# Kernel tuning notes

Hardware: AMD Instinct MI355X
Metric: run time of the kernel (lower is better)

## Reference

```python
import jax, jax.numpy as jnp
import numpy as np

B, N_CAM, D_BINS, HF, WF, C = 1, 6, 118, 32, 88, 80
DZ, DY, DX = 1, 128, 128
N_POINTS = 1_000_000
BEV_FEAT_SHAPE = (B, DZ, DY, DX, C)  # (B, Dz, Dy, Dx, C)


def setup_inputs() -> dict:
    key = jax.random.key(0)
    k1, k2, k3, k4, k5 = jax.random.split(key, 5)
    depth = jax.random.uniform(k1, (B, N_CAM, D_BINS, HF, WF), dtype=jnp.float32)
    feat = jax.random.normal(k2, (B, N_CAM, HF, WF, C), dtype=jnp.float32)
    n_depth = B * N_CAM * D_BINS * HF * WF      # flattened depth size
    n_feat_rows = B * N_CAM * HF * WF           # rows of flattened feat
    n_bev = B * DZ * DY * DX                    # flattened BEV grid size
    ranks_depths = jax.random.randint(k3, (N_POINTS,), 0, n_depth, dtype=jnp.int32)
    ranks_feats = jax.random.randint(k4, (N_POINTS,), 0, n_feat_rows, dtype=jnp.int32)
    ranks_bevs = jnp.sort(jax.random.randint(k5, (N_POINTS,), 0, n_bev, dtype=jnp.int32))
    # intervals consistent with sorted ranks_bevs (contiguous runs of equal bev rank)
    rb = np.asarray(ranks_bevs)
    change = np.concatenate([[True], rb[1:] != rb[:-1]])
    starts = np.flatnonzero(change)
    lengths = np.diff(np.append(starts, len(rb)))
    return {
        "depth": depth,
        "feat": feat,
        "ranks_depths": ranks_depths,
        "ranks_feats": ranks_feats,
        "ranks_bevs": ranks_bevs,
        "bev_feat_shape": BEV_FEAT_SHAPE,
        "interval_starts": jnp.asarray(starts, dtype=jnp.int32),
        "interval_lengths": jnp.asarray(lengths, dtype=jnp.int32),
    }


def reference(depth, feat, ranks_depths, ranks_feats, ranks_bevs,
              bev_feat_shape, interval_starts, interval_lengths):
    # bev_pool_v2: gather depth scalar and feat row per point, multiply,
    # scatter-sum into the BEV grid. Interval-based summation over sorted
    # ranks_bevs is mathematically a segment-sum keyed by ranks_bevs, so we
    # use segment_sum directly (intervals are redundant metadata).
    b, dz, dy, dx, c = bev_feat_shape
    d = depth.reshape(-1)[ranks_depths]               # [P]
    f = feat.reshape(-1, c)[ranks_feats]              # [P, C]
    out = jax.ops.segment_sum(f * d[:, None], ranks_bevs,
                              num_segments=b * dz * dy * dx)  # [B*Dz*Dy*Dx, C]
    out = out.reshape(b, dz, dy, dx, c)
    return jnp.transpose(out, (0, 4, 1, 2, 3))        # (B, C, Dz, Dy, Dx)
```

## Files before the change

kernel.cpp:

```cpp
#include <hip/hip_runtime.h>
#include <hip/hip_bf16.h>


#define C_CH   80
#define QPT    20
#define SPLITS 8
#define IPB    2
#define BLOCK  (IPB * QPT * SPLITS)

__global__ __launch_bounds__(BLOCK) void bev_pool_split_kernel(
    const float*  __restrict__ depth,
    const float4* __restrict__ feat4,
    const int*    __restrict__ rd,
    const int*    __restrict__ rf,
    const int*    __restrict__ rb,
    const int*    __restrict__ istart,
    const int*    __restrict__ ilen,
    int n_intervals,
    int n_bev,
    float* __restrict__ out)
{
    __shared__ float4 red[IPB][SPLITS][QPT];

    int tid   = threadIdx.x;
    int il    = tid / (QPT * SPLITS);
    int r     = tid - il * (QPT * SPLITS);
    int split = r / QPT;
    int quad  = r - split * QPT;
    int interval = blockIdx.x * IPB + il;
    bool valid = interval < n_intervals;

    float4 acc = make_float4(0.f, 0.f, 0.f, 0.f);
    int start = 0, len = 0, bev = 0;

    if (valid) {
        start = istart[interval];
        len   = ilen[interval];
        bev   = rb[start];

        int i = split;
        for (; i + SPLITS < len; i += 2 * SPLITS) {
            int p0 = start + i;
            int p1 = p0 + SPLITS;
            int rd0 = rd[p0], rf0 = rf[p0];
            int rd1 = rd[p1], rf1 = rf[p1];
            float d0 = depth[rd0];
            float d1 = depth[rd1];
            float4 f0 = feat4[(long)rf0 * QPT + quad];
            float4 f1 = feat4[(long)rf1 * QPT + quad];
            acc.x += d0 * f0.x; acc.y += d0 * f0.y;
            acc.z += d0 * f0.z; acc.w += d0 * f0.w;
            acc.x += d1 * f1.x; acc.y += d1 * f1.y;
            acc.z += d1 * f1.z; acc.w += d1 * f1.w;
        }
        if (i < len) {
            int p = start + i;
            float d = depth[rd[p]];
            float4 f = feat4[(long)rf[p] * QPT + quad];
            acc.x += d * f.x; acc.y += d * f.y;
            acc.z += d * f.z; acc.w += d * f.w;
        }
    }

    red[il][split][quad] = acc;
    __syncthreads();

    if (valid && split == 0) {
        float4 s = acc;
        #pragma unroll
        for (int k = 1; k < SPLITS; ++k) {
            float4 t = red[il][k][quad];
            s.x += t.x; s.y += t.y; s.z += t.z; s.w += t.w;
        }
        long o = (long)(quad * 4) * n_bev + bev;
        out[o]             = s.x;
        out[o + n_bev]     = s.y;
        out[o + 2L * n_bev] = s.z;
        out[o + 3L * n_bev] = s.w;
    }
}

extern "C" void kernel_launch(void* const* d_in, const int* in_sizes, int n_in,
                              void* d_out, int out_size, void* d_ws, size_t ws_size,
                              hipStream_t stream) {
    const float*  depth = (const float*)d_in[0];
    const float4* feat4 = (const float4*)d_in[1];
    const int* ranks_depth = (const int*)d_in[2];
    const int* ranks_feat  = (const int*)d_in[3];
    const int* ranks_bev   = (const int*)d_in[4];
    const int* interval_starts  = (const int*)d_in[6];
    const int* interval_lengths = (const int*)d_in[7];

    int n_intervals = in_sizes[6];
    int n_bev = out_size / C_CH;
    float* out = (float*)d_out;

    hipMemsetAsync(d_out, 0, (size_t)out_size * sizeof(float), stream);

    int grid = (n_intervals + IPB - 1) / IPB;
    bev_pool_split_kernel<<<grid, BLOCK, 0, stream>>>(
        depth, feat4, ranks_depth, ranks_feat, ranks_bev,
        interval_starts, interval_lengths, n_intervals, n_bev, out);
}
```

Before: 134.9 us.

## Pre-gather depth values and split channels across blocks in clustered grid

Adds a separate kernel that gathers depth values per point into a contiguous workspace buffer, so the main kernel reads them coalesced instead of doing a dependent random gather. The main kernel now splits the 80 channels into two halves handled by different blocks, with 4 intervals per block. Blocks are arranged in clusters of 8 so that neighbouring blocks share intervals and can reuse index data through cache. This adds an extra kernel launch and a P-sized write and read, and it duplicates the index and depth reads across the two channel halves.

```diff
diff --git a/kernel.cpp b/kernel.cpp
--- a/kernel.cpp
+++ b/kernel.cpp
@@ -4,14 +4,25 @@
 
 #define C_CH   80
 #define QPT    20
+#define HQ     10
 #define SPLITS 8
-#define IPB    2
-#define BLOCK  (IPB * QPT * SPLITS)
+#define IPB    4
+#define BLOCK  (IPB * SPLITS * HQ)
+#define CLUST  (IPB * 4)
 
-__global__ __launch_bounds__(BLOCK) void bev_pool_split_kernel(
+__global__ void depth_gather_kernel(const float* __restrict__ depth,
+                                    const int*   __restrict__ rd,
+                                    float* __restrict__ dgath, int P) {
+    int i = blockIdx.x * blockDim.x + threadIdx.x;
+    if (i < P) dgath[i] = depth[rd[i]];
+}
+
+template <bool USE_DG>
+__global__ __launch_bounds__(BLOCK) void bev_pool_main_kernel(
     const float*  __restrict__ depth,
+    const float*  __restrict__ dgath,
+    const int*    __restrict__ rd,
     const float4* __restrict__ feat4,
-    const int*    __restrict__ rd,
     const int*    __restrict__ rf,
     const int*    __restrict__ rb,
     const int*    __restrict__ istart,
@@ -20,34 +31,42 @@
     int n_bev,
     float* __restrict__ out)
 {
-    __shared__ float4 red[IPB][SPLITS][QPT];
+    __shared__ float4 red[IPB][SPLITS][HQ];
+
+    int bid     = blockIdx.x;
+    int slot    = bid & 7;
+    int cluster = bid >> 3;
+    int half    = slot >> 2;
+    int quarter = slot & 3;
+    int ibase   = cluster * CLUST + quarter * IPB;
 
     int tid   = threadIdx.x;
-    int il    = tid / (QPT * SPLITS);
-    int r     = tid - il * (QPT * SPLITS);
-    int split = r / QPT;
-    int quad  = r - split * QPT;
-    int interval = blockIdx.x * IPB + il;
+    int il    = tid / (SPLITS * HQ);
+    int r     = tid - il * (SPLITS * HQ);
+    int split = r / HQ;
+    int q     = r - split * HQ;
+    int gq    = half * HQ + q;
+
+    int interval = ibase + il;
     bool valid = interval < n_intervals;
 
     float4 acc = make_float4(0.f, 0.f, 0.f, 0.f);
-    int start = 0, len = 0, bev = 0;
+    int bev = 0;
 
     if (valid) {
-        start = istart[interval];
-        len   = ilen[interval];
-        bev   = rb[start];
+        int start = istart[interval];
+        int len   = ilen[interval];
+        bev = rb[start];
 
         int i = split;
         for (; i + SPLITS < len; i += 2 * SPLITS) {
             int p0 = start + i;
             int p1 = p0 + SPLITS;
-            int rd0 = rd[p0], rf0 = rf[p0];
-            int rd1 = rd[p1], rf1 = rf[p1];
-            float d0 = depth[rd0];
-            float d1 = depth[rd1];
-            float4 f0 = feat4[(long)rf0 * QPT + quad];
-            float4 f1 = feat4[(long)rf1 * QPT + quad];
+            float d0 = USE_DG ? dgath[p0] : depth[rd[p0]];
+            float d1 = USE_DG ? dgath[p1] : depth[rd[p1]];
+            int rf0 = rf[p0], rf1 = rf[p1];
+            float4 f0 = feat4[(long)rf0 * QPT + gq];
+            float4 f1 = feat4[(long)rf1 * QPT + gq];
             acc.x += d0 * f0.x; acc.y += d0 * f0.y;
             acc.z += d0 * f0.z; acc.w += d0 * f0.w;
             acc.x += d1 * f1.x; acc.y += d1 * f1.y;
@@ -55,26 +74,26 @@
         }
         if (i < len) {
             int p = start + i;
-            float d = depth[rd[p]];
-            float4 f = feat4[(long)rf[p] * QPT + quad];
+            float d = USE_DG ? dgath[p] : depth[rd[p]];
+            float4 f = feat4[(long)rf[p] * QPT + gq];
             acc.x += d * f.x; acc.y += d * f.y;
             acc.z += d * f.z; acc.w += d * f.w;
         }
     }
 
-    red[il][split][quad] = acc;
+    red[il][split][q] = acc;
     __syncthreads();
 
     if (valid && split == 0) {
         float4 s = acc;
         #pragma unroll
         for (int k = 1; k < SPLITS; ++k) {
-            float4 t = red[il][k][quad];
+            float4 t = red[il][k][q];
             s.x += t.x; s.y += t.y; s.z += t.z; s.w += t.w;
         }
-        long o = (long)(quad * 4) * n_bev + bev;
-        out[o]             = s.x;
-        out[o + n_bev]     = s.y;
+        long o = (long)(gq * 4) * n_bev + bev;
+        out[o]              = s.x;
+        out[o + n_bev]      = s.y;
         out[o + 2L * n_bev] = s.z;
         out[o + 3L * n_bev] = s.w;
     }
@@ -91,14 +110,30 @@
     const int* interval_starts  = (const int*)d_in[6];
     const int* interval_lengths = (const int*)d_in[7];
 
+    int P = in_sizes[2];
     int n_intervals = in_sizes[6];
     int n_bev = out_size / C_CH;
     float* out = (float*)d_out;
+    float* dgath = (float*)d_ws;
 
     hipMemsetAsync(d_out, 0, (size_t)out_size * sizeof(float), stream);
 
-    int grid = (n_intervals + IPB - 1) / IPB;
-    bev_pool_split_kernel<<<grid, BLOCK, 0, stream>>>(
-        depth, feat4, ranks_depth, ranks_feat, ranks_bev,
-        interval_starts, interval_lengths, n_intervals, n_bev, out);
+    bool use_dg = ws_size >= (size_t)P * sizeof(float);
+    if (use_dg) {
+        int gblock = 256;
+        int ggrid = (P + gblock - 1) / gblock;
+        depth_gather_kernel<<<ggrid, gblock, 0, stream>>>(depth, ranks_depth, dgath, P);
+    }
+
+    int clusters = (n_intervals + CLUST - 1) / CLUST;
+    int grid = clusters * 8;
+    if (use_dg) {
+        bev_pool_main_kernel<true><<<grid, BLOCK, 0, stream>>>(
+            depth, dgath, ranks_depth, feat4, ranks_feat, ranks_bev,
+            interval_starts, interval_lengths, n_intervals, n_bev, out);
+    } else {
+        bev_pool_main_kernel<false><<<grid, BLOCK, 0, stream>>>(
+            depth, dgath, ranks_depth, feat4, ranks_feat, ranks_bev,
+            interval_starts, interval_lengths, n_intervals, n_bev, out);
+    }
 }
```

Result: no change. 133.7 us (-0.9%).

## Pre-convert features to bf16 and pre-gather depth in a prep kernel

Applied to the files above, without the earlier changes.

Adds a prep kernel that rounds the feature tensor to packed bf16 and gathers the depth value for each point into a contiguous workspace array. The main kernel then reads 16-byte bf16 chunks of 8 channels per lane and the pre-gathered depths, with 10 lanes per point and 4 intervals per block. The aim is to halve random feature-gather traffic and take the dependent depth gather out of the inner loop. The cost is an extra pass over feat and ranks_depths and a loss of feature precision to bf16; the old fp32 path remains as a fallback when the workspace is too small.

```diff
diff --git a/kernel.cpp b/kernel.cpp
--- a/kernel.cpp
+++ b/kernel.cpp
@@ -3,15 +3,53 @@
 
 
 #define C_CH   80
-#define QPT    20
+#define NL     10
 #define SPLITS 8
-#define IPB    2
-#define BLOCK  (IPB * QPT * SPLITS)
+#define IPB    4
+#define BLOCK  (IPB * SPLITS * NL)
 
-__global__ __launch_bounds__(BLOCK) void bev_pool_split_kernel(
+__global__ void prep_kernel(const float*  __restrict__ depth,
+                            const int*    __restrict__ rd,
+                            const float4* __restrict__ feat4,
+                            float* __restrict__ dgath,
+                            uint2* __restrict__ fbf,
+                            int P, int NF4) {
+    int i = blockIdx.x * blockDim.x + threadIdx.x;
+    if (i < NF4) {
+        float4 v = feat4[i];
+        float f[4] = {v.x, v.y, v.z, v.w};
+        unsigned h[4];
+        #pragma unroll
+        for (int k = 0; k < 4; ++k) {
+            unsigned u = __float_as_uint(f[k]);
+            h[k] = (u + 0x7fffu + ((u >> 16) & 1u)) >> 16;
+        }
+        uint2 o;
+        o.x = h[0] | (h[1] << 16);
+        o.y = h[2] | (h[3] << 16);
+        fbf[i] = o;
+    }
+    if (i < P) dgath[i] = depth[rd[i]];
+}
+
+__device__ __forceinline__ void bf8_fma(float acc[8], float d, int4 w) {
+    unsigned v[4] = {(unsigned)w.x, (unsigned)w.y, (unsigned)w.z, (unsigned)w.w};
+    #pragma unroll
+    for (int k = 0; k < 4; ++k) {
+        float lo = __uint_as_float(v[k] << 16);
+        float hi = __uint_as_float(v[k] & 0xffff0000u);
+        acc[2 * k]     += d * lo;
+        acc[2 * k + 1] += d * hi;
+    }
+}
+
+template <bool FAST>
+__global__ __launch_bounds__(BLOCK) void bev_main(
     const float*  __restrict__ depth,
-    const float4* __restrict__ feat4,
     const int*    __restrict__ rd,
+    const float*  __restrict__ dgath,
+    const int4*   __restrict__ fbf,
+    const float4* __restrict__ featf,
     const int*    __restrict__ rf,
     const int*    __restrict__ rb,
     const int*    __restrict__ istart,
@@ -20,63 +58,84 @@
     int n_bev,
     float* __restrict__ out)
 {
-    __shared__ float4 red[IPB][SPLITS][QPT];
+    __shared__ float red[IPB][SPLITS][NL][9];
 
     int tid   = threadIdx.x;
-    int il    = tid / (QPT * SPLITS);
-    int r     = tid - il * (QPT * SPLITS);
-    int split = r / QPT;
-    int quad  = r - split * QPT;
+    int il    = tid / (SPLITS * NL);
+    int r     = tid - il * (SPLITS * NL);
+    int split = r / NL;
+    int l10   = r - split * NL;
     int interval = blockIdx.x * IPB + il;
     bool valid = interval < n_intervals;
 
-    float4 acc = make_float4(0.f, 0.f, 0.f, 0.f);
-    int start = 0, len = 0, bev = 0;
+    float acc[8] = {0.f, 0.f, 0.f, 0.f, 0.f, 0.f, 0.f, 0.f};
+    int bev = 0;
 
     if (valid) {
-        start = istart[interval];
-        len   = ilen[interval];
-        bev   = rb[start];
+        int start = istart[interval];
+        int len   = ilen[interval];
+        bev = rb[start];
 
         int i = split;
         for (; i + SPLITS < len; i += 2 * SPLITS) {
             int p0 = start + i;
             int p1 = p0 + SPLITS;
-            int rd0 = rd[p0], rf0 = rf[p0];
-            int rd1 = rd[p1], rf1 = rf[p1];
-            float d0 = depth[rd0];
-            float d1 = depth[rd1];
-            float4 f0 = feat4[(long)rf0 * QPT + quad];
-            float4 f1 = feat4[(long)rf1 * QPT + quad];
-            acc.x += d0 * f0.x; acc.y += d0 * f0.y;
-            acc.z += d0 * f0.z; acc.w += d0 * f0.w;
-            acc.x += d1 * f1.x; acc.y += d1 * f1.y;
-            acc.z += d1 * f1.z; acc.w += d1 * f1.w;
+            float d0 = FAST ? dgath[p0] : depth[rd[p0]];
+            float d1 = FAST ? dgath[p1] : depth[rd[p1]];
+            int q0 = rf[p0], q1 = rf[p1];
+            if (FAST) {
+                int4 w0 = fbf[(long)q0 * NL + l10];
+                int4 w1 = fbf[(long)q1 * NL + l10];
+                bf8_fma(acc, d0, w0);
+                bf8_fma(acc, d1, w1);
+            } else {
+                float4 a0 = featf[(long)q0 * 20 + l10 * 2];
+                float4 a1 = featf[(long)q0 * 20 + l10 * 2 + 1];
+                float4 b0 = featf[(long)q1 * 20 + l10 * 2];
+                float4 b1 = featf[(long)q1 * 20 + l10 * 2 + 1];
+                acc[0] += d0 * a0.x; acc[1] += d0 * a0.y;
+                acc[2] += d0 * a0.z; acc[3] += d0 * a0.w;
+                acc[4] += d0 * a1.x; acc[5] += d0 * a1.y;
+                acc[6] += d0 * a1.z; acc[7] += d0 * a1.w;
+                acc[0] += d1 * b0.x; acc[1] += d1 * b0.y;
+                acc[2] += d1 * b0.z; acc[3] += d1 * b0.w;
+                acc[4] += d1 * b1.x; acc[5] += d1 * b1.y;
+                acc[6] += d1 * b1.z; acc[7] += d1 * b1.w;
+            }
         }
-        if (i < len) {
+        for (; i < len; i += SPLITS) {
             int p = start + i;
-            float d = depth[rd[p]];
-            float4 f = feat4[(long)rf[p] * QPT + quad];
-            acc.x += d * f.x; acc.y += d * f.y;
-            acc.z += d * f.z; acc.w += d * f.w;
+            float d = FAST ? dgath[p] : depth[rd[p]];
+            int q = rf[p];
+            if (FAST) {
+                bf8_fma(acc, d, fbf[(long)q * NL + l10]);
+            } else {
+                float4 a0 = featf[(long)q * 20 + l10 * 2];
+                float4 a1 = featf[(long)q * 20 + l10 * 2 + 1];
+                acc[0] += d * a0.x; acc[1] += d * a0.y;
+                acc[2] += d * a0.z; acc[3] += d * a0.w;
+                acc[4] += d * a1.x; acc[5] += d * a1.y;
+                acc[6] += d * a1.z; acc[7] += d * a1.w;
+            }
         }
     }
 
-    red[il][split][quad] = acc;
+    #pragma unroll
+    for (int j = 0; j < 8; ++j) red[il][split][l10][j] = acc[j];
     __syncthreads();
 
     if (valid && split == 0) {
-        float4 s = acc;
+        float s[8];
+        #pragma unroll
+        for (int j = 0; j < 8; ++j) s[j] = acc[j];
         #pragma unroll
         for (int k = 1; k < SPLITS; ++k) {
-            float4 t = red[il][k][quad];
-            s.x += t.x; s.y += t.y; s.z += t.z; s.w += t.w;
+            #pragma unroll
+            for (int j = 0; j < 8; ++j) s[j] += red[il][k][l10][j];
         }
-        long o = (long)(quad * 4) * n_bev + bev;
-        out[o]             = s.x;
-        out[o + n_bev]     = s.y;
-        out[o + 2L * n_bev] = s.z;
-        out[o + 3L * n_bev] = s.w;
+        long ob = (long)(l10 * 8) * n_bev + bev;
+        #pragma unroll
+        for (int j = 0; j < 8; ++j) out[ob + (long)j * n_bev] = s[j];
     }
 }
 
@@ -91,14 +150,40 @@
     const int* interval_starts  = (const int*)d_in[6];
     const int* interval_lengths = (const int*)d_in[7];
 
+    int P   = in_sizes[2];
+    int NF  = in_sizes[1];
+    int NF4 = NF / 4;
     int n_intervals = in_sizes[6];
     int n_bev = out_size / C_CH;
     float* out = (float*)d_out;
 
+    size_t dg_bytes  = ((size_t)P * sizeof(float) + 15) & ~(size_t)15;
+    size_t fbf_bytes = (size_t)NF * 2;
+    bool fast = ws_size >= dg_bytes + fbf_bytes;
+
+    float* dgath = (float*)d_ws;
+    uint2* fbf   = (uint2*)((char*)d_ws + dg_bytes);
+
     hipMemsetAsync(d_out, 0, (size_t)out_size * sizeof(float), stream);
 
+    if (fast) {
+        int n = P > NF4 ? P : NF4;
+        int gblock = 256;
+        int ggrid = (n + gblock - 1) / gblock;
+        prep_kernel<<<ggrid, gblock, 0, stream>>>(depth, ranks_depth, feat4,
+                                                  dgath, fbf, P, NF4);
+    }
+
     int grid = (n_intervals + IPB - 1) / IPB;
-    bev_pool_split_kernel<<<grid, BLOCK, 0, stream>>>(
-        depth, feat4, ranks_depth, ranks_feat, ranks_bev,
-        interval_starts, interval_lengths, n_intervals, n_bev, out);
+    if (fast) {
+        bev_main<true><<<grid, BLOCK, 0, stream>>>(
+            depth, ranks_depth, dgath, (const int4*)fbf, feat4,
+            ranks_feat, ranks_bev, interval_starts, interval_lengths,
+            n_intervals, n_bev, out);
+    } else {
+        bev_main<false><<<grid, BLOCK, 0, stream>>>(
+            depth, ranks_depth, dgath, (const int4*)fbf, feat4,
+            ranks_feat, ranks_bev, interval_starts, interval_lengths,
+            n_intervals, n_bev, out);
+    }
 }
```

Measured after the change: 118.1 us (median of 2 runs). 1.14x faster.
